# Performance work log

Hardware: AMD Instinct MI355X
Metric: run time of the kernel (lower is better)

Reference implementation:

```python
import jax, jax.numpy as jnp
import numpy as np

B, S, I, H = 128, 1024, 512, 512


def _masked_linear(x, W, Wm):
    # 'feat'-wise MaskedLinear: sigmoid(x @ Wm^T) * (x @ W^T); no bias.
    return jax.nn.sigmoid(x @ Wm.T) * (x @ W.T)


def setup_inputs() -> dict:
    key = jax.random.key(0)
    keys = jax.random.split(key, 24)
    stdv = 1.0 / np.sqrt(H)
    u = lambda k, shape: jax.random.uniform(k, shape, jnp.float32, -stdv, stdv)
    names_W = ["Wf", "Wf_m", "Wi", "Wi_m", "Wo", "Wo_m", "Wc", "Wc_m"]
    names_U = ["Uf", "Uf_m", "Ui", "Ui_m", "Uo", "Uo_m", "Uc", "Uc_m"]
    d = {}
    for j, n in enumerate(names_W):
        d[n] = u(keys[j], (H, I))
    for j, n in enumerate(names_U):
        d[n] = u(keys[8 + j], (H, H))
    for j, n in enumerate(["bf", "bi", "bo", "bc"]):
        d[n] = u(keys[16 + j], (H,))
    d["x"] = jax.random.normal(keys[20], (B, S, I), jnp.float32)
    return d


def reference(x, Wf, Wf_m, Wi, Wi_m, Wo, Wo_m, Wc, Wc_m,
              Uf, Uf_m, Ui, Ui_m, Uo, Uo_m, Uc, Uc_m,
              bf, bi, bo, bc):
    batch = x.shape[0]
    h0 = jnp.zeros((batch, H), x.dtype)
    c0 = jnp.zeros((batch, H), x.dtype)

    def step(carry, x_t):
        h, c = carry
        f = jax.nn.sigmoid(_masked_linear(x_t, Wf, Wf_m) + _masked_linear(h, Uf, Uf_m) + bf)
        i = jax.nn.sigmoid(_masked_linear(x_t, Wi, Wi_m) + _masked_linear(h, Ui, Ui_m) + bi)  # unused (bug in original, reproduced)
        o = jax.nn.sigmoid(_masked_linear(x_t, Wo, Wo_m) + _masked_linear(h, Uo, Uo_m) + bo)
        c = f * c + jnp.tanh(_masked_linear(x_t, Wc, Wc_m) + _masked_linear(h, Uc, Uc_m) + bc)
        h = o * c
        return (h, c), h

    (hT, cT), ys = jax.lax.scan(step, (h0, c0), jnp.swapaxes(x, 0, 1))  # ys: [S,B,H]
    output = jnp.swapaxes(ys, 0, 1)  # [B,S,H]
    # original returns h,c of shape [n_layers*dirs=1, B, H]
    return output, (hT[None], cT[None])
```

## Files before the change

kernel.cpp:

```cpp
#include <hip/hip_runtime.h>
#include <hip/hip_bf16.h>


typedef __attribute__((ext_vector_type(8))) short short8;
typedef __attribute__((ext_vector_type(4))) float floatx4;
typedef unsigned short ushort_t;

static constexpr size_t kMat   = 512 * 512;
static constexpr size_t O_W    = 0;
static constexpr size_t O_XGO  = 12 * kMat * 2;
static constexpr size_t O_XGC  = O_XGO + 134217728ull;
static constexpr size_t O_XGF  = O_XGC + 134217728ull;
static constexpr size_t O_HB   = O_XGF + 131072ull;

__device__ __forceinline__ ushort_t f2bf(float f) {
  unsigned u = __float_as_uint(f);
  u = (u + 0x7FFFu + ((u >> 16) & 1u)) >> 16;
  return (ushort_t)u;
}
__device__ __forceinline__ float bf2f(ushort_t h) {
  return __uint_as_float(((unsigned)h) << 16);
}
__device__ __forceinline__ float sigf(float x) { return 1.0f / (1.0f + __expf(-x)); }
__device__ __forceinline__ float tanhfast(float x) { return 2.0f * sigf(2.0f * x) - 1.0f; }

struct Ptrs12 { const float* p[12]; };

__global__ void k_prep(Ptrs12 a, ushort_t* __restrict__ wbf, unsigned* __restrict__ zr) {
  unsigned idx = blockIdx.x * 256u + threadIdx.x;
  const unsigned WTOT = 12u * 262144u;
  if (idx < WTOT) {
    wbf[idx] = f2bf(a.p[idx >> 18][idx & 262143u]);
  } else {
    zr[idx - WTOT] = 0u;
  }
}

__global__ __launch_bounds__(256, 2) void k_xgemm(
    const float* __restrict__ x, const ushort_t* __restrict__ wbf,
    ushort_t* __restrict__ xgo, ushort_t* __restrict__ xgc,
    ushort_t* __restrict__ xgf_last, ushort_t* out_xgf) {
  __shared__ ushort_t At[128][64];
  __shared__ ushort_t Bt[2][128][64];
  const int combo = blockIdx.x;
  const int p  = combo % 3;
  const int n0 = (combo / 3) * 128;
  const int R0 = blockIdx.y * 128;
  const ushort_t* Wmain = wbf + (size_t)(2 * p) * kMat;
  const ushort_t* Wmask = wbf + (size_t)(2 * p + 1) * kMat;
  const int tid = threadIdx.x;
  const int lane = tid & 63, w = tid >> 6;
  const int wr = w >> 1, wc = w & 1;
  const int sr = tid >> 1, sh = tid & 1;

  floatx4 accM[4][4], accK[4][4];
#pragma unroll
  for (int mt = 0; mt < 4; ++mt)
#pragma unroll
    for (int nt = 0; nt < 4; ++nt) {
      accM[mt][nt] = (floatx4){0.f, 0.f, 0.f, 0.f};
      accK[mt][nt] = (floatx4){0.f, 0.f, 0.f, 0.f};
    }

  for (int kb = 0; kb < 8; ++kb) {
    __syncthreads();
    const float* xa = x + (size_t)(R0 + sr) * 512 + kb * 64 + sh * 32;
#pragma unroll
    for (int q = 0; q < 4; ++q) {
      float4 v0 = *reinterpret_cast<const float4*>(xa + q * 8);
      float4 v1 = *reinterpret_cast<const float4*>(xa + q * 8 + 4);
      short8 s;
      s[0] = (short)f2bf(v0.x); s[1] = (short)f2bf(v0.y);
      s[2] = (short)f2bf(v0.z); s[3] = (short)f2bf(v0.w);
      s[4] = (short)f2bf(v1.x); s[5] = (short)f2bf(v1.y);
      s[6] = (short)f2bf(v1.z); s[7] = (short)f2bf(v1.w);
      *reinterpret_cast<short8*>(&At[sr][sh * 32 + q * 8]) = s;
    }
#pragma unroll
    for (int m2 = 0; m2 < 2; ++m2) {
      const ushort_t* src = (m2 ? Wmask : Wmain) + (size_t)(n0 + sr) * 512 + kb * 64 + sh * 32;
#pragma unroll
      for (int q = 0; q < 4; ++q)
        *reinterpret_cast<short8*>(&Bt[m2][sr][sh * 32 + q * 8]) =
            *reinterpret_cast<const short8*>(src + q * 8);
    }
    __syncthreads();
#pragma unroll
    for (int ks = 0; ks < 2; ++ks) {
      const int ko = ks * 32 + (lane >> 4) * 8;
      short8 a[4], b0[4], b1[4];
#pragma unroll
      for (int mt = 0; mt < 4; ++mt)
        a[mt] = *reinterpret_cast<const short8*>(&At[wr * 64 + mt * 16 + (lane & 15)][ko]);
#pragma unroll
      for (int nt = 0; nt < 4; ++nt) {
        b0[nt] = *reinterpret_cast<const short8*>(&Bt[0][wc * 64 + nt * 16 + (lane & 15)][ko]);
        b1[nt] = *reinterpret_cast<const short8*>(&Bt[1][wc * 64 + nt * 16 + (lane & 15)][ko]);
      }
#pragma unroll
      for (int mt = 0; mt < 4; ++mt)
#pragma unroll
        for (int nt = 0; nt < 4; ++nt) {
          accM[mt][nt] = __builtin_amdgcn_mfma_f32_16x16x32_bf16(a[mt], b0[nt], accM[mt][nt], 0, 0, 0);
          accK[mt][nt] = __builtin_amdgcn_mfma_f32_16x16x32_bf16(a[mt], b1[nt], accK[mt][nt], 0, 0, 0);
        }
    }
  }
#pragma unroll
  for (int mt = 0; mt < 4; ++mt)
#pragma unroll
    for (int nt = 0; nt < 4; ++nt)
#pragma unroll
      for (int r = 0; r < 4; ++r) {
        float val = sigf(accK[mt][nt][r]) * accM[mt][nt][r];
        int row = R0 + wr * 64 + mt * 16 + (lane >> 4) * 4 + r;
        int col = n0 + wc * 64 + nt * 16 + (lane & 15);
        ushort_t bv = f2bf(val);
        if (p == 1) {
          xgo[(size_t)row * 512 + col] = bv;
        } else if (p == 2) {
          xgc[(size_t)row * 512 + col] = bv;
        } else {
          int t = row & 1023;
          if (t == 1023) xgf_last[(row >> 10) * 512 + col] = bv;
          else out_xgf[(size_t)(row + 1) * 1024 + 512 + col] = bv;
        }
      }
}

__global__ __launch_bounds__(256, 1) void k_recur(
    const ushort_t* __restrict__ ubf,
    const ushort_t* __restrict__ xgo, const ushort_t* __restrict__ xgc,
    const ushort_t* __restrict__ xgf_last,
    unsigned* hbuf,
    const float* __restrict__ bfp, const float* __restrict__ bop, const float* __restrict__ bcp,
    float* out) {
  __shared__ ushort_t htile[16][520];
  __shared__ float comb[12][8][16];
  const int bid = blockIdx.x;
  const int team = bid >> 4;
  const int member = bid & 15;
  const int tid = threadIdx.x;
  const int lane = tid & 63, w = tid >> 6;

  short8 uw[3][16];
#pragma unroll
  for (int i = 0; i < 3; ++i) {
    const int c = w + 4 * i;
    const int m = c % 6, ct = c / 6;
    const int row = member * 32 + ct * 16 + (lane & 15);
    const ushort_t* src = ubf + (size_t)m * kMat + (size_t)row * 512 + (lane >> 4) * 8;
#pragma unroll
    for (int kf = 0; kf < 16; ++kf)
      uw[i][kf] = *reinterpret_cast<const short8*>(src + kf * 32);
  }
#pragma unroll
  for (int i = 0; i < 3; ++i)
#pragma unroll
    for (int kf = 0; kf < 16; ++kf)
      asm volatile("" : "+v"(uw[i][kf]));

  {
    unsigned* hrow = reinterpret_cast<unsigned*>(&htile[8 + (tid >> 5)][0]) + (tid & 31) * 8;
#pragma unroll
    for (int q = 0; q < 8; ++q) hrow[q] = 0u;
    if (tid < 64) {
      reinterpret_cast<unsigned*>(&htile[tid >> 2][512])[tid & 3] = 0u;
    }
  }

  const int er = tid >> 5;
  const int ej = tid & 31;
  const int ect = ej >> 4, ejj = ej & 15;
  const int col = member * 32 + ej;
  const int b = team * 8 + er;
  const float bfv = bfp[col], bov = bop[col], bcv = bcp[col];
  float cp = 0.0f;

  unsigned* hb = hbuf + (size_t)team * 8192;
  const ushort_t* out_us = reinterpret_cast<const ushort_t*>(out);

  for (int t = 0; t < 1024; ++t) {
    const size_t bt = (size_t)b * 1024 + t;
    const float xov = bf2f(xgo[bt * 512 + col]);
    const float xcv = bf2f(xgc[bt * 512 + col]);
    const float xfv = (t == 1023) ? bf2f(xgf_last[b * 512 + col])
                                  : bf2f(out_us[(bt + 1) * 1024 + 512 + col]);

    {
      const unsigned tg = (unsigned)t & 0xFFFFu;
      const unsigned* src = hb + (size_t)(t & 1) * 4096 + tid;
      unsigned wv[16];
      if (t) __builtin_amdgcn_s_sleep(8);
#pragma unroll
      for (int q = 0; q < 16; ++q)
        wv[q] = __hip_atomic_load(src + q * 256, __ATOMIC_RELAXED, __HIP_MEMORY_SCOPE_AGENT);
      for (;;) {
        unsigned bad = 0u;
#pragma unroll
        for (int q = 0; q < 16; ++q) bad |= (wv[q] ^ tg);
        if ((bad & 0xFFFFu) == 0u) break;
#pragma unroll
        for (int q = 0; q < 16; ++q)
          if ((wv[q] & 0xFFFFu) != tg)
            wv[q] = __hip_atomic_load(src + q * 256, __ATOMIC_RELAXED, __HIP_MEMORY_SCOPE_AGENT);
      }
#pragma unroll
      for (int q = 0; q < 16; ++q)
        htile[q >> 1][(q & 1) * 256 + tid] = (ushort_t)(wv[q] >> 16);
    }
    __syncthreads();

    short8 af[16];
    {
      const ushort_t* abase = &htile[lane & 15][(lane >> 4) * 8];
#pragma unroll
      for (int kf = 0; kf < 16; ++kf)
        af[kf] = *reinterpret_cast<const short8*>(abase + kf * 32);
    }

    floatx4 acc[3];
#pragma unroll
    for (int i = 0; i < 3; ++i) acc[i] = (floatx4){0.f, 0.f, 0.f, 0.f};
#pragma unroll
    for (int kf = 0; kf < 16; ++kf)
#pragma unroll
      for (int i = 0; i < 3; ++i)
        acc[i] = __builtin_amdgcn_mfma_f32_16x16x32_bf16(af[kf], uw[i][kf], acc[i], 0, 0, 0);

    if (lane < 32) {
      const int rr = (lane >> 4) * 4;
#pragma unroll
      for (int i = 0; i < 3; ++i) {
        const int c = w + 4 * i;
#pragma unroll
        for (int r = 0; r < 4; ++r) comb[c][rr + r][lane & 15] = acc[i][r];
      }
    }
    __syncthreads();

    const float hUf  = comb[ect * 6 + 0][er][ejj];
    const float hUfm = comb[ect * 6 + 1][er][ejj];
    const float hUo  = comb[ect * 6 + 2][er][ejj];
    const float hUom = comb[ect * 6 + 3][er][ejj];
    const float hUc  = comb[ect * 6 + 4][er][ejj];
    const float hUcm = comb[ect * 6 + 5][er][ejj];

    const float fg = sigf(sigf(hUfm) * hUf + xfv + bfv);
    const float og = sigf(sigf(hUom) * hUo + xov + bov);
    const float cn = fg * cp + tanhfast(sigf(hUcm) * hUc + xcv + bcv);
    const float hv = og * cn;
    cp = cn;

    if (t < 1023) {
      const unsigned word = ((unsigned)f2bf(hv) << 16) | ((unsigned)(t + 1) & 0xFFFFu);
      __hip_atomic_store(hb + (size_t)((t + 1) & 1) * 4096 + er * 512 + col, word,
                         __ATOMIC_RELAXED, __HIP_MEMORY_SCOPE_AGENT);
    }

    out[bt * 512 + col] = hv;
    if (t == 1023) {
      out[67108864ull + (size_t)b * 512 + col] = hv;
      out[67108864ull + 65536ull + (size_t)b * 512 + col] = cn;
    }
    __syncthreads();
  }
}

extern "C" void kernel_launch(void* const* d_in, const int* in_sizes, int n_in,
                              void* d_out, int out_size, void* d_ws, size_t ws_size,
                              hipStream_t stream) {
  (void)in_sizes; (void)n_in; (void)out_size; (void)ws_size;
  char* ws = (char*)d_ws;
  ushort_t* wbf = (ushort_t*)(ws + O_W);
  const ushort_t* ubf = wbf + 6 * kMat;
  ushort_t* xgo = (ushort_t*)(ws + O_XGO);
  ushort_t* xgc = (ushort_t*)(ws + O_XGC);
  ushort_t* xgfl = (ushort_t*)(ws + O_XGF);
  unsigned* hbuf = (unsigned*)(ws + O_HB);

  Ptrs12 pa;
  pa.p[0] = (const float*)d_in[0];  pa.p[1] = (const float*)d_in[1];
  pa.p[2] = (const float*)d_in[4];  pa.p[3] = (const float*)d_in[5];
  pa.p[4] = (const float*)d_in[6];  pa.p[5] = (const float*)d_in[7];
  pa.p[6] = (const float*)d_in[8];  pa.p[7] = (const float*)d_in[9];
  pa.p[8] = (const float*)d_in[12]; pa.p[9] = (const float*)d_in[13];
  pa.p[10] = (const float*)d_in[14]; pa.p[11] = (const float*)d_in[15];

  hipLaunchKernelGGL(k_prep, dim3((12u * 262144u + 131072u) / 256u), dim3(256), 0, stream,
                     pa, wbf, hbuf);
  hipLaunchKernelGGL(k_xgemm, dim3(12, 1024), dim3(256), 0, stream,
                     (const float*)d_in[20], wbf, xgo, xgc, xgfl, (ushort_t*)d_out);

  const ushort_t* a_ubf = ubf;
  const ushort_t* a_xgo = xgo;
  const ushort_t* a_xgc = xgc;
  const ushort_t* a_xgfl = xgfl;
  unsigned* a_hbuf = hbuf;
  const float* a_bf = (const float*)d_in[16];
  const float* a_bo = (const float*)d_in[18];
  const float* a_bc = (const float*)d_in[19];
  float* a_out = (float*)d_out;
  void* kargs[9] = { (void*)&a_ubf, (void*)&a_xgo, (void*)&a_xgc, (void*)&a_xgfl,
                     (void*)&a_hbuf, (void*)&a_bf, (void*)&a_bo, (void*)&a_bc, (void*)&a_out };
  hipError_t ce = hipLaunchCooperativeKernel((const void*)k_recur, dim3(256), dim3(256),
                                             kargs, 0, stream);
  if (ce != hipSuccess) {
    hipLaunchKernelGGL(k_recur, dim3(256), dim3(256), 0, stream,
                       ubf, xgo, xgc, xgfl, hbuf, a_bf, a_bo, a_bc, a_out);
  }
}
```

Baseline: 3.392 ms.

## Split batch rows into two half-groups to overlap h exchange with MFMA

The recurrent step now processes the 8 batch rows as two groups of 4. Each group waits only on its own half of the shared hidden-state buffer, so one half's MFMA and gate math can overlap with polling for the other half. The next step's first-half loads are issued early and the s_sleep is removed. The cost is two MFMA passes per step with zero-padded rows, which doubles matrix-unit work, plus an extra barrier round per step.

After: 5.023 ms. 48.1% more time.

```diff
diff --git a/kernel.cpp b/kernel.cpp
--- a/kernel.cpp
+++ b/kernel.cpp
@@ -161,17 +161,15 @@
       asm volatile("" : "+v"(uw[i][kf]));
 
   {
-    unsigned* hrow = reinterpret_cast<unsigned*>(&htile[8 + (tid >> 5)][0]) + (tid & 31) * 8;
-#pragma unroll
-    for (int q = 0; q < 8; ++q) hrow[q] = 0u;
-    if (tid < 64) {
-      reinterpret_cast<unsigned*>(&htile[tid >> 2][512])[tid & 3] = 0u;
-    }
+    unsigned* hz = reinterpret_cast<unsigned*>(&htile[0][0]);
+    for (int q = tid; q < 4160; q += 256) hz[q] = 0u;
   }
 
   const int er = tid >> 5;
   const int ej = tid & 31;
   const int ect = ej >> 4, ejj = ej & 15;
+  const int g_my = er >> 2;
+  const int lr = er & 3;
   const int col = member * 32 + ej;
   const int b = team * 8 + er;
   const float bfv = bfp[col], bov = bop[col], bcv = bcp[col];
@@ -179,6 +177,16 @@
 
   unsigned* hb = hbuf + (size_t)team * 8192;
   const ushort_t* out_us = reinterpret_cast<const ushort_t*>(out);
+
+  unsigned wv0[8], wv1[8];
+  {
+    const unsigned* s0 = hb + tid;
+#pragma unroll
+    for (int q = 0; q < 8; ++q)
+      wv0[q] = __hip_atomic_load(s0 + q * 256, __ATOMIC_RELAXED, __HIP_MEMORY_SCOPE_AGENT);
+    __builtin_amdgcn_sched_barrier(0);
+  }
+  __syncthreads();
 
   for (int t = 0; t < 1024; ++t) {
     const size_t bt = (size_t)b * 1024 + t;
@@ -186,84 +194,151 @@
     const float xcv = bf2f(xgc[bt * 512 + col]);
     const float xfv = (t == 1023) ? bf2f(xgf_last[b * 512 + col])
                                   : bf2f(out_us[(bt + 1) * 1024 + 512 + col]);
+    const unsigned tg = (unsigned)t & 0xFFFFu;
 
     {
-      const unsigned tg = (unsigned)t & 0xFFFFu;
-      const unsigned* src = hb + (size_t)(t & 1) * 4096 + tid;
-      unsigned wv[16];
-      if (t) __builtin_amdgcn_s_sleep(8);
-#pragma unroll
-      for (int q = 0; q < 16; ++q)
-        wv[q] = __hip_atomic_load(src + q * 256, __ATOMIC_RELAXED, __HIP_MEMORY_SCOPE_AGENT);
+      const unsigned* s0 = hb + (size_t)(t & 1) * 4096 + tid;
       for (;;) {
         unsigned bad = 0u;
 #pragma unroll
-        for (int q = 0; q < 16; ++q) bad |= (wv[q] ^ tg);
+        for (int q = 0; q < 8; ++q) bad |= (wv0[q] ^ tg);
         if ((bad & 0xFFFFu) == 0u) break;
 #pragma unroll
-        for (int q = 0; q < 16; ++q)
-          if ((wv[q] & 0xFFFFu) != tg)
-            wv[q] = __hip_atomic_load(src + q * 256, __ATOMIC_RELAXED, __HIP_MEMORY_SCOPE_AGENT);
-      }
-#pragma unroll
-      for (int q = 0; q < 16; ++q)
-        htile[q >> 1][(q & 1) * 256 + tid] = (ushort_t)(wv[q] >> 16);
-    }
-    __syncthreads();
-
-    short8 af[16];
+        for (int q = 0; q < 8; ++q)
+          if ((wv0[q] & 0xFFFFu) != tg)
+            wv0[q] = __hip_atomic_load(s0 + q * 256, __ATOMIC_RELAXED, __HIP_MEMORY_SCOPE_AGENT);
+      }
+      const unsigned* s1 = hb + (size_t)(t & 1) * 4096 + 2048 + tid;
+#pragma unroll
+      for (int q = 0; q < 8; ++q)
+        wv1[q] = __hip_atomic_load(s1 + q * 256, __ATOMIC_RELAXED, __HIP_MEMORY_SCOPE_AGENT);
+      __builtin_amdgcn_sched_barrier(0);
+#pragma unroll
+      for (int q = 0; q < 8; ++q)
+        htile[q >> 1][(q & 1) * 256 + tid] = (ushort_t)(wv0[q] >> 16);
+    }
+    __syncthreads();
     {
+      short8 af[16];
       const ushort_t* abase = &htile[lane & 15][(lane >> 4) * 8];
 #pragma unroll
       for (int kf = 0; kf < 16; ++kf)
         af[kf] = *reinterpret_cast<const short8*>(abase + kf * 32);
-    }
-
-    floatx4 acc[3];
-#pragma unroll
-    for (int i = 0; i < 3; ++i) acc[i] = (floatx4){0.f, 0.f, 0.f, 0.f};
-#pragma unroll
-    for (int kf = 0; kf < 16; ++kf)
-#pragma unroll
-      for (int i = 0; i < 3; ++i)
-        acc[i] = __builtin_amdgcn_mfma_f32_16x16x32_bf16(af[kf], uw[i][kf], acc[i], 0, 0, 0);
-
-    if (lane < 32) {
-      const int rr = (lane >> 4) * 4;
-#pragma unroll
-      for (int i = 0; i < 3; ++i) {
-        const int c = w + 4 * i;
-#pragma unroll
-        for (int r = 0; r < 4; ++r) comb[c][rr + r][lane & 15] = acc[i][r];
-      }
-    }
-    __syncthreads();
-
-    const float hUf  = comb[ect * 6 + 0][er][ejj];
-    const float hUfm = comb[ect * 6 + 1][er][ejj];
-    const float hUo  = comb[ect * 6 + 2][er][ejj];
-    const float hUom = comb[ect * 6 + 3][er][ejj];
-    const float hUc  = comb[ect * 6 + 4][er][ejj];
-    const float hUcm = comb[ect * 6 + 5][er][ejj];
-
-    const float fg = sigf(sigf(hUfm) * hUf + xfv + bfv);
-    const float og = sigf(sigf(hUom) * hUo + xov + bov);
-    const float cn = fg * cp + tanhfast(sigf(hUcm) * hUc + xcv + bcv);
-    const float hv = og * cn;
-    cp = cn;
-
-    if (t < 1023) {
-      const unsigned word = ((unsigned)f2bf(hv) << 16) | ((unsigned)(t + 1) & 0xFFFFu);
-      __hip_atomic_store(hb + (size_t)((t + 1) & 1) * 4096 + er * 512 + col, word,
-                         __ATOMIC_RELAXED, __HIP_MEMORY_SCOPE_AGENT);
-    }
-
-    out[bt * 512 + col] = hv;
-    if (t == 1023) {
-      out[67108864ull + (size_t)b * 512 + col] = hv;
-      out[67108864ull + 65536ull + (size_t)b * 512 + col] = cn;
-    }
-    __syncthreads();
+      floatx4 acc[3];
+#pragma unroll
+      for (int i = 0; i < 3; ++i) acc[i] = (floatx4){0.f, 0.f, 0.f, 0.f};
+#pragma unroll
+      for (int kf = 0; kf < 16; ++kf)
+#pragma unroll
+        for (int i = 0; i < 3; ++i)
+          acc[i] = __builtin_amdgcn_mfma_f32_16x16x32_bf16(af[kf], uw[i][kf], acc[i], 0, 0, 0);
+      if (lane < 32) {
+        const int rr = (lane >> 4) * 4;
+#pragma unroll
+        for (int i = 0; i < 3; ++i) {
+          const int c = w + 4 * i;
+#pragma unroll
+          for (int r = 0; r < 4; ++r) comb[c][rr + r][lane & 15] = acc[i][r];
+        }
+      }
+    }
+    __syncthreads();
+    if (g_my == 0) {
+      const float hUf  = comb[ect * 6 + 0][lr][ejj];
+      const float hUfm = comb[ect * 6 + 1][lr][ejj];
+      const float hUo  = comb[ect * 6 + 2][lr][ejj];
+      const float hUom = comb[ect * 6 + 3][lr][ejj];
+      const float hUc  = comb[ect * 6 + 4][lr][ejj];
+      const float hUcm = comb[ect * 6 + 5][lr][ejj];
+      const float fg = sigf(sigf(hUfm) * hUf + xfv + bfv);
+      const float og = sigf(sigf(hUom) * hUo + xov + bov);
+      const float cn = fg * cp + tanhfast(sigf(hUcm) * hUc + xcv + bcv);
+      const float hv = og * cn;
+      cp = cn;
+      if (t < 1023) {
+        const unsigned word = ((unsigned)f2bf(hv) << 16) | ((unsigned)(t + 1) & 0xFFFFu);
+        __hip_atomic_store(hb + (size_t)((t + 1) & 1) * 4096 + er * 512 + col, word,
+                           __ATOMIC_RELAXED, __HIP_MEMORY_SCOPE_AGENT);
+      }
+      out[bt * 512 + col] = hv;
+      if (t == 1023) {
+        out[67108864ull + (size_t)b * 512 + col] = hv;
+        out[67108864ull + 65536ull + (size_t)b * 512 + col] = cp;
+      }
+    }
+
+    {
+      const unsigned* s1 = hb + (size_t)(t & 1) * 4096 + 2048 + tid;
+      for (;;) {
+        unsigned bad = 0u;
+#pragma unroll
+        for (int q = 0; q < 8; ++q) bad |= (wv1[q] ^ tg);
+        if ((bad & 0xFFFFu) == 0u) break;
+#pragma unroll
+        for (int q = 0; q < 8; ++q)
+          if ((wv1[q] & 0xFFFFu) != tg)
+            wv1[q] = __hip_atomic_load(s1 + q * 256, __ATOMIC_RELAXED, __HIP_MEMORY_SCOPE_AGENT);
+      }
+      if (t < 1023) {
+        const unsigned* s0n = hb + (size_t)((t + 1) & 1) * 4096 + tid;
+#pragma unroll
+        for (int q = 0; q < 8; ++q)
+          wv0[q] = __hip_atomic_load(s0n + q * 256, __ATOMIC_RELAXED, __HIP_MEMORY_SCOPE_AGENT);
+        __builtin_amdgcn_sched_barrier(0);
+      }
+#pragma unroll
+      for (int q = 0; q < 8; ++q)
+        htile[q >> 1][(q & 1) * 256 + tid] = (ushort_t)(wv1[q] >> 16);
+    }
+    __syncthreads();
+    {
+      short8 af[16];
+      const ushort_t* abase = &htile[lane & 15][(lane >> 4) * 8];
+#pragma unroll
+      for (int kf = 0; kf < 16; ++kf)
+        af[kf] = *reinterpret_cast<const short8*>(abase + kf * 32);
+      floatx4 acc[3];
+#pragma unroll
+      for (int i = 0; i < 3; ++i) acc[i] = (floatx4){0.f, 0.f, 0.f, 0.f};
+#pragma unroll
+      for (int kf = 0; kf < 16; ++kf)
+#pragma unroll
+        for (int i = 0; i < 3; ++i)
+          acc[i] = __builtin_amdgcn_mfma_f32_16x16x32_bf16(af[kf], uw[i][kf], acc[i], 0, 0, 0);
+      if (lane < 32) {
+        const int rr = (lane >> 4) * 4;
+#pragma unroll
+        for (int i = 0; i < 3; ++i) {
+          const int c = w + 4 * i;
+#pragma unroll
+          for (int r = 0; r < 4; ++r) comb[c][rr + r][lane & 15] = acc[i][r];
+        }
+      }
+    }
+    __syncthreads();
+    if (g_my == 1) {
+      const float hUf  = comb[ect * 6 + 0][lr][ejj];
+      const float hUfm = comb[ect * 6 + 1][lr][ejj];
+      const float hUo  = comb[ect * 6 + 2][lr][ejj];
+      const float hUom = comb[ect * 6 + 3][lr][ejj];
+      const float hUc  = comb[ect * 6 + 4][lr][ejj];
+      const float hUcm = comb[ect * 6 + 5][lr][ejj];
+      const float fg = sigf(sigf(hUfm) * hUf + xfv + bfv);
+      const float og = sigf(sigf(hUom) * hUo + xov + bov);
+      const float cn = fg * cp + tanhfast(sigf(hUcm) * hUc + xcv + bcv);
+      const float hv = og * cn;
+      cp = cn;
+      if (t < 1023) {
+        const unsigned word = ((unsigned)f2bf(hv) << 16) | ((unsigned)(t + 1) & 0xFFFFu);
+        __hip_atomic_store(hb + (size_t)((t + 1) & 1) * 4096 + er * 512 + col, word,
+                           __ATOMIC_RELAXED, __HIP_MEMORY_SCOPE_AGENT);
+      }
+      out[bt * 512 + col] = hv;
+      if (t == 1023) {
+        out[67108864ull + (size_t)b * 512 + col] = hv;
+        out[67108864ull + 65536ull + (size_t)b * 512 + col] = cp;
+      }
+    }
   }
 }
 
```

## Interleave two independent batch teams per block to hide inter-block sync latency

Applied to the files above, without the earlier changes.

Each recurrent block now handles two batch teams, A and B, and alternates between them within every timestep, so the grid shrinks from 256 to 128 blocks. The h-exchange loads for one team are issued before the other team's compute. The aim is for the cross-block polling latency of each team to overlap the other team's MFMA and gate work. In exchange, each block does twice the serial work per step with half the CUs in use, and more registers are held for prefetched words.

Result: slower. 5.882 ms (+73.4%).

```diff
diff --git a/kernel.cpp b/kernel.cpp
--- a/kernel.cpp
+++ b/kernel.cpp
@@ -138,7 +138,8 @@
   __shared__ ushort_t htile[16][520];
   __shared__ float comb[12][8][16];
   const int bid = blockIdx.x;
-  const int team = bid >> 4;
+  const int teamA = bid >> 4;
+  const int teamB = teamA + 8;
   const int member = bid & 15;
   const int tid = threadIdx.x;
   const int lane = tid & 63, w = tid >> 6;
@@ -173,97 +174,183 @@
   const int ej = tid & 31;
   const int ect = ej >> 4, ejj = ej & 15;
   const int col = member * 32 + ej;
-  const int b = team * 8 + er;
+  const int bA = teamA * 8 + er;
+  const int bB = teamB * 8 + er;
   const float bfv = bfp[col], bov = bop[col], bcv = bcp[col];
-  float cp = 0.0f;
-
-  unsigned* hb = hbuf + (size_t)team * 8192;
+  float cpA = 0.0f, cpB = 0.0f;
+
+  unsigned* hbA = hbuf + (size_t)teamA * 8192;
+  unsigned* hbB = hbuf + (size_t)teamB * 8192;
   const ushort_t* out_us = reinterpret_cast<const ushort_t*>(out);
 
+  unsigned wvA[16], wvB[16];
+  {
+    const unsigned* s0 = hbA + tid;
+#pragma unroll
+    for (int q = 0; q < 16; ++q)
+      wvA[q] = __hip_atomic_load(s0 + q * 256, __ATOMIC_RELAXED, __HIP_MEMORY_SCOPE_AGENT);
+    __builtin_amdgcn_sched_barrier(0);
+  }
+  __syncthreads();
+
   for (int t = 0; t < 1024; ++t) {
-    const size_t bt = (size_t)b * 1024 + t;
-    const float xov = bf2f(xgo[bt * 512 + col]);
-    const float xcv = bf2f(xgc[bt * 512 + col]);
-    const float xfv = (t == 1023) ? bf2f(xgf_last[b * 512 + col])
-                                  : bf2f(out_us[(bt + 1) * 1024 + 512 + col]);
-
-    {
-      const unsigned tg = (unsigned)t & 0xFFFFu;
-      const unsigned* src = hb + (size_t)(t & 1) * 4096 + tid;
-      unsigned wv[16];
-      if (t) __builtin_amdgcn_s_sleep(8);
+    const unsigned tg = (unsigned)t & 0xFFFFu;
+
+    {
+      const unsigned* sB = hbB + (size_t)(t & 1) * 4096 + tid;
 #pragma unroll
       for (int q = 0; q < 16; ++q)
-        wv[q] = __hip_atomic_load(src + q * 256, __ATOMIC_RELAXED, __HIP_MEMORY_SCOPE_AGENT);
+        wvB[q] = __hip_atomic_load(sB + q * 256, __ATOMIC_RELAXED, __HIP_MEMORY_SCOPE_AGENT);
+      __builtin_amdgcn_sched_barrier(0);
+    }
+    const size_t btA = (size_t)bA * 1024 + t;
+    const float xovA = bf2f(xgo[btA * 512 + col]);
+    const float xcvA = bf2f(xgc[btA * 512 + col]);
+    const float xfvA = (t == 1023) ? bf2f(xgf_last[bA * 512 + col])
+                                   : bf2f(out_us[(btA + 1) * 1024 + 512 + col]);
+    {
+      const unsigned* sA = hbA + (size_t)(t & 1) * 4096 + tid;
       for (;;) {
         unsigned bad = 0u;
 #pragma unroll
-        for (int q = 0; q < 16; ++q) bad |= (wv[q] ^ tg);
+        for (int q = 0; q < 16; ++q) bad |= (wvA[q] ^ tg);
         if ((bad & 0xFFFFu) == 0u) break;
 #pragma unroll
         for (int q = 0; q < 16; ++q)
-          if ((wv[q] & 0xFFFFu) != tg)
-            wv[q] = __hip_atomic_load(src + q * 256, __ATOMIC_RELAXED, __HIP_MEMORY_SCOPE_AGENT);
+          if ((wvA[q] & 0xFFFFu) != tg)
+            wvA[q] = __hip_atomic_load(sA + q * 256, __ATOMIC_RELAXED, __HIP_MEMORY_SCOPE_AGENT);
       }
 #pragma unroll
       for (int q = 0; q < 16; ++q)
-        htile[q >> 1][(q & 1) * 256 + tid] = (ushort_t)(wv[q] >> 16);
-    }
-    __syncthreads();
-
-    short8 af[16];
-    {
+        htile[q >> 1][(q & 1) * 256 + tid] = (ushort_t)(wvA[q] >> 16);
+    }
+    __syncthreads();
+    {
+      short8 af[16];
       const ushort_t* abase = &htile[lane & 15][(lane >> 4) * 8];
 #pragma unroll
       for (int kf = 0; kf < 16; ++kf)
         af[kf] = *reinterpret_cast<const short8*>(abase + kf * 32);
-    }
-
-    floatx4 acc[3];
-#pragma unroll
-    for (int i = 0; i < 3; ++i) acc[i] = (floatx4){0.f, 0.f, 0.f, 0.f};
-#pragma unroll
-    for (int kf = 0; kf < 16; ++kf)
-#pragma unroll
-      for (int i = 0; i < 3; ++i)
-        acc[i] = __builtin_amdgcn_mfma_f32_16x16x32_bf16(af[kf], uw[i][kf], acc[i], 0, 0, 0);
-
-    if (lane < 32) {
-      const int rr = (lane >> 4) * 4;
-#pragma unroll
-      for (int i = 0; i < 3; ++i) {
-        const int c = w + 4 * i;
-#pragma unroll
-        for (int r = 0; r < 4; ++r) comb[c][rr + r][lane & 15] = acc[i][r];
-      }
-    }
-    __syncthreads();
-
-    const float hUf  = comb[ect * 6 + 0][er][ejj];
-    const float hUfm = comb[ect * 6 + 1][er][ejj];
-    const float hUo  = comb[ect * 6 + 2][er][ejj];
-    const float hUom = comb[ect * 6 + 3][er][ejj];
-    const float hUc  = comb[ect * 6 + 4][er][ejj];
-    const float hUcm = comb[ect * 6 + 5][er][ejj];
-
-    const float fg = sigf(sigf(hUfm) * hUf + xfv + bfv);
-    const float og = sigf(sigf(hUom) * hUo + xov + bov);
-    const float cn = fg * cp + tanhfast(sigf(hUcm) * hUc + xcv + bcv);
-    const float hv = og * cn;
-    cp = cn;
-
+      floatx4 acc[3];
+#pragma unroll
+      for (int i = 0; i < 3; ++i) acc[i] = (floatx4){0.f, 0.f, 0.f, 0.f};
+#pragma unroll
+      for (int kf = 0; kf < 16; ++kf)
+#pragma unroll
+        for (int i = 0; i < 3; ++i)
+          acc[i] = __builtin_amdgcn_mfma_f32_16x16x32_bf16(af[kf], uw[i][kf], acc[i], 0, 0, 0);
+      if (lane < 32) {
+        const int rr = (lane >> 4) * 4;
+#pragma unroll
+        for (int i = 0; i < 3; ++i) {
+          const int c = w + 4 * i;
+#pragma unroll
+          for (int r = 0; r < 4; ++r) comb[c][rr + r][lane & 15] = acc[i][r];
+        }
+      }
+    }
+    __syncthreads();
+    {
+      const float hUf  = comb[ect * 6 + 0][er][ejj];
+      const float hUfm = comb[ect * 6 + 1][er][ejj];
+      const float hUo  = comb[ect * 6 + 2][er][ejj];
+      const float hUom = comb[ect * 6 + 3][er][ejj];
+      const float hUc  = comb[ect * 6 + 4][er][ejj];
+      const float hUcm = comb[ect * 6 + 5][er][ejj];
+      const float fg = sigf(sigf(hUfm) * hUf + xfvA + bfv);
+      const float og = sigf(sigf(hUom) * hUo + xovA + bov);
+      const float cn = fg * cpA + tanhfast(sigf(hUcm) * hUc + xcvA + bcv);
+      const float hv = og * cn;
+      cpA = cn;
+      if (t < 1023) {
+        const unsigned word = ((unsigned)f2bf(hv) << 16) | ((unsigned)(t + 1) & 0xFFFFu);
+        __hip_atomic_store(hbA + (size_t)((t + 1) & 1) * 4096 + er * 512 + col, word,
+                           __ATOMIC_RELAXED, __HIP_MEMORY_SCOPE_AGENT);
+      }
+      out[btA * 512 + col] = hv;
+      if (t == 1023) {
+        out[67108864ull + (size_t)bA * 512 + col] = hv;
+        out[67108864ull + 65536ull + (size_t)bA * 512 + col] = cn;
+      }
+    }
+
+    const size_t btB = (size_t)bB * 1024 + t;
+    const float xovB = bf2f(xgo[btB * 512 + col]);
+    const float xcvB = bf2f(xgc[btB * 512 + col]);
+    const float xfvB = (t == 1023) ? bf2f(xgf_last[bB * 512 + col])
+                                   : bf2f(out_us[(btB + 1) * 1024 + 512 + col]);
+    {
+      const unsigned* sB = hbB + (size_t)(t & 1) * 4096 + tid;
+      for (;;) {
+        unsigned bad = 0u;
+#pragma unroll
+        for (int q = 0; q < 16; ++q) bad |= (wvB[q] ^ tg);
+        if ((bad & 0xFFFFu) == 0u) break;
+#pragma unroll
+        for (int q = 0; q < 16; ++q)
+          if ((wvB[q] & 0xFFFFu) != tg)
+            wvB[q] = __hip_atomic_load(sB + q * 256, __ATOMIC_RELAXED, __HIP_MEMORY_SCOPE_AGENT);
+      }
+#pragma unroll
+      for (int q = 0; q < 16; ++q)
+        htile[q >> 1][(q & 1) * 256 + tid] = (ushort_t)(wvB[q] >> 16);
+    }
+    __syncthreads();
     if (t < 1023) {
-      const unsigned word = ((unsigned)f2bf(hv) << 16) | ((unsigned)(t + 1) & 0xFFFFu);
-      __hip_atomic_store(hb + (size_t)((t + 1) & 1) * 4096 + er * 512 + col, word,
-                         __ATOMIC_RELAXED, __HIP_MEMORY_SCOPE_AGENT);
-    }
-
-    out[bt * 512 + col] = hv;
-    if (t == 1023) {
-      out[67108864ull + (size_t)b * 512 + col] = hv;
-      out[67108864ull + 65536ull + (size_t)b * 512 + col] = cn;
-    }
-    __syncthreads();
+      const unsigned* sA = hbA + (size_t)((t + 1) & 1) * 4096 + tid;
+#pragma unroll
+      for (int q = 0; q < 16; ++q)
+        wvA[q] = __hip_atomic_load(sA + q * 256, __ATOMIC_RELAXED, __HIP_MEMORY_SCOPE_AGENT);
+      __builtin_amdgcn_sched_barrier(0);
+    }
+    {
+      short8 af[16];
+      const ushort_t* abase = &htile[lane & 15][(lane >> 4) * 8];
+#pragma unroll
+      for (int kf = 0; kf < 16; ++kf)
+        af[kf] = *reinterpret_cast<const short8*>(abase + kf * 32);
+      floatx4 acc[3];
+#pragma unroll
+      for (int i = 0; i < 3; ++i) acc[i] = (floatx4){0.f, 0.f, 0.f, 0.f};
+#pragma unroll
+      for (int kf = 0; kf < 16; ++kf)
+#pragma unroll
+        for (int i = 0; i < 3; ++i)
+          acc[i] = __builtin_amdgcn_mfma_f32_16x16x32_bf16(af[kf], uw[i][kf], acc[i], 0, 0, 0);
+      if (lane < 32) {
+        const int rr = (lane >> 4) * 4;
+#pragma unroll
+        for (int i = 0; i < 3; ++i) {
+          const int c = w + 4 * i;
+#pragma unroll
+          for (int r = 0; r < 4; ++r) comb[c][rr + r][lane & 15] = acc[i][r];
+        }
+      }
+    }
+    __syncthreads();
+    {
+      const float hUf  = comb[ect * 6 + 0][er][ejj];
+      const float hUfm = comb[ect * 6 + 1][er][ejj];
+      const float hUo  = comb[ect * 6 + 2][er][ejj];
+      const float hUom = comb[ect * 6 + 3][er][ejj];
+      const float hUc  = comb[ect * 6 + 4][er][ejj];
+      const float hUcm = comb[ect * 6 + 5][er][ejj];
+      const float fg = sigf(sigf(hUfm) * hUf + xfvB + bfv);
+      const float og = sigf(sigf(hUom) * hUo + xovB + bov);
+      const float cn = fg * cpB + tanhfast(sigf(hUcm) * hUc + xcvB + bcv);
+      const float hv = og * cn;
+      cpB = cn;
+      if (t < 1023) {
+        const unsigned word = ((unsigned)f2bf(hv) << 16) | ((unsigned)(t + 1) & 0xFFFFu);
+        __hip_atomic_store(hbB + (size_t)((t + 1) & 1) * 4096 + er * 512 + col, word,
+                           __ATOMIC_RELAXED, __HIP_MEMORY_SCOPE_AGENT);
+      }
+      out[btB * 512 + col] = hv;
+      if (t == 1023) {
+        out[67108864ull + (size_t)bB * 512 + col] = hv;
+        out[67108864ull + 65536ull + (size_t)bB * 512 + col] = cn;
+      }
+    }
   }
 }
 
@@ -303,10 +390,10 @@
   float* a_out = (float*)d_out;
   void* kargs[9] = { (void*)&a_ubf, (void*)&a_xgo, (void*)&a_xgc, (void*)&a_xgfl,
                      (void*)&a_hbuf, (void*)&a_bf, (void*)&a_bo, (void*)&a_bc, (void*)&a_out };
-  hipError_t ce = hipLaunchCooperativeKernel((const void*)k_recur, dim3(256), dim3(256),
+  hipError_t ce = hipLaunchCooperativeKernel((const void*)k_recur, dim3(128), dim3(256),
                                              kargs, 0, stream);
   if (ce != hipSuccess) {
-    hipLaunchKernelGGL(k_recur, dim3(256), dim3(256), 0, stream,
+    hipLaunchKernelGGL(k_recur, dim3(128), dim3(256), 0, stream,
                        ubf, xgo, xgc, xgfl, hbuf, a_bf, a_bo, a_bc, a_out);
   }
 }
```
